# Optimization experiments

Measured on AMD Instinct MI355X. Metric: run time of the kernel, lower is better.

The kernel has to match this reference:

```python
import jax, jax.numpy as jnp
import numpy as np

S, B, D, H, A = 256, 1024, 64, 128, 8  # seq_len, buffer, state_size, hidden, action_size


def _init(key, shape, fan_in):
    bound = 1.0 / np.sqrt(fan_in)
    return jax.random.uniform(key, shape, jnp.float32, -bound, bound)


def setup_inputs() -> dict:
    key = jax.random.key(0)
    ks = jax.random.split(key, 24)
    inp = {"state": jax.random.normal(ks[0], (S, B, D), jnp.float32)}
    # actor / critic MLPs (Linear(D,H) + ReLU + Linear(H,H) + ReLU)
    inp["aw1"] = _init(ks[1], (H, D), D); inp["ab1"] = _init(ks[2], (H,), D)
    inp["aw2"] = _init(ks[3], (H, H), H); inp["ab2"] = _init(ks[4], (H,), H)
    inp["cw1"] = _init(ks[5], (H, D), D); inp["cb1"] = _init(ks[6], (H,), D)
    inp["cw2"] = _init(ks[7], (H, H), H); inp["cb2"] = _init(ks[8], (H,), H)
    # LSTMs (PyTorch layout: W_ih [4H,H], W_hh [4H,H], gate order i,f,g,o)
    inp["a_wih"] = _init(ks[9], (4 * H, H), H); inp["a_whh"] = _init(ks[10], (4 * H, H), H)
    inp["a_bih"] = _init(ks[11], (4 * H,), H); inp["a_bhh"] = _init(ks[12], (4 * H,), H)
    inp["c_wih"] = _init(ks[13], (4 * H, H), H); inp["c_whh"] = _init(ks[14], (4 * H, H), H)
    inp["c_bih"] = _init(ks[15], (4 * H,), H); inp["c_bhh"] = _init(ks[16], (4 * H,), H)
    # heads
    inp["mw"] = _init(ks[17], (A, H), H); inp["mb"] = _init(ks[18], (A,), H)
    inp["lw"] = _init(ks[19], (A, H), H); inp["lb"] = _init(ks[20], (A,), H)
    inp["vw"] = _init(ks[21], (1, H), H); inp["vb"] = _init(ks[22], (1,), H)
    return inp


def _mlp(x, w1, b1, w2, b2):
    h = jax.nn.relu(jnp.einsum('sbd,hd->sbh', x, w1) + b1)
    return jax.nn.relu(jnp.einsum('sbh,gh->sbg', h, w2) + b2)


def _lstm_zero_state(x, w_ih, b_ih, b_hh):
    # Each timestep runs with fresh zero (h, c): the recurrent term vanishes,
    # so the whole sequence is one batched GEMM + gating (W_hh unused).
    gates = jnp.einsum('sbh,gh->sbg', x, w_ih) + b_ih + b_hh  # [S,B,4H]
    i, f, g, o = jnp.split(gates, 4, axis=-1)
    c = jax.nn.sigmoid(i) * jnp.tanh(g)  # f * c_prev = 0
    return jax.nn.sigmoid(o) * jnp.tanh(c)


def reference(state, aw1, ab1, aw2, ab2, cw1, cb1, cw2, cb2,
              a_wih, a_whh, a_bih, a_bhh, c_wih, c_whh, c_bih, c_bhh,
              mw, mb, lw, lb, vw, vb):
    actor_h = _lstm_zero_state(_mlp(state, aw1, ab1, aw2, ab2), a_wih, a_bih, a_bhh)
    critic_h = _lstm_zero_state(_mlp(state, cw1, cb1, cw2, cb2), c_wih, c_bih, c_bhh)
    mean = jnp.einsum('sbh,ah->sba', actor_h, mw) + mb
    std = jnp.exp(jnp.einsum('sbh,ah->sba', actor_h, lw) + lb)
    value = jnp.einsum('sbh,vh->sbv', critic_h, vw) + vb
    return (mean, std, value)
```

## Files before the change

kernel.cpp:

```cpp
#include <hip/hip_runtime.h>


#define NROWS (256 * 1024)
#define HID 128
#define ACTD 8

#define W1_OFF 0
#define W2_OFF 16384
#define WI_OFF 49152
#define WG_OFF 81920
#define WO_OFF 114688
#define PSTR 147456
#define HEAD_OFF (2 * PSTR)
#define GB_OFF (HEAD_OFF + 8192)

#define NEG_L (-1.4426950408889634f)
#define TWO_L (2.8853900817779268f)

typedef __attribute__((ext_vector_type(8))) short s16x8;
typedef __attribute__((ext_vector_type(4))) float fx4;
typedef __attribute__((ext_vector_type(2))) unsigned int u32x2;
typedef __attribute__((ext_vector_type(4))) unsigned int u32x4;

__device__ __forceinline__ unsigned int cvtpk(float lo, float hi) {
  unsigned int r;
  asm("v_cvt_pk_bf16_f32 %0, %1, %2" : "=v"(r) : "v"(lo), "v"(hi));
  return r;
}

__device__ __forceinline__ float ex2(float x) {
  return __builtin_amdgcn_exp2f(x);
}
__device__ __forceinline__ float frcp(float x) {
  return __builtin_amdgcn_rcpf(x);
}

__device__ __forceinline__ s16x8 frag_ld(const unsigned short* base, int row,
                                         int kbyte, int rowsh) {
  int byte = (row << rowsh) + (kbyte ^ ((row & 7) << 4));
  return *(const s16x8*)((const char*)base + byte);
}

__device__ __forceinline__ void zacc(fx4 acc[4][2]) {
#pragma unroll
  for (int j = 0; j < 4; ++j)
#pragma unroll
    for (int i = 0; i < 2; ++i) acc[j][i] = fx4{0.f, 0.f, 0.f, 0.f};
}

__device__ __forceinline__ void bacc(fx4 acc[4][2], const float* __restrict__ b,
                                     int fb, int g4) {
#pragma unroll
  for (int it = 0; it < 2; ++it) {
    fx4 bv = *(const fx4*)(b + fb + it * 16 + g4);
#pragma unroll
    for (int jt = 0; jt < 4; ++jt) acc[jt][it] = bv;
  }
}

template <int KC, int ASH>
__device__ __forceinline__ void gemm_g(const char* __restrict__ wimg,
                                       const unsigned short* at, int wv,
                                       int lane, fx4 acc[4][2]) {
  const int l15 = lane & 15;
  const int kb0 = (lane >> 4) << 4;
  const int woff = ((lane >> 4) << 8) + (l15 << 4);
#pragma unroll
  for (int kc = 0; kc < KC; ++kc) {
    int kbyte = kc * 64 + kb0;
    s16x8 w0 = *(const s16x8*)(wimg + (((wv * 2 + 0) * KC + kc) << 10) + woff);
    s16x8 w1 = *(const s16x8*)(wimg + (((wv * 2 + 1) * KC + kc) << 10) + woff);
#pragma unroll
    for (int jt = 0; jt < 4; ++jt) {
      s16x8 a = frag_ld(at, jt * 16 + l15, kbyte, ASH);
      acc[jt][0] = __builtin_amdgcn_mfma_f32_16x16x32_bf16(w0, a, acc[jt][0], 0, 0, 0);
      acc[jt][1] = __builtin_amdgcn_mfma_f32_16x16x32_bf16(w1, a, acc[jt][1], 0, 0, 0);
    }
  }
}

__device__ __forceinline__ void epi_relu(fx4 acc[4][2], unsigned short* obuf,
                                         int fb, int lane) {
  const int g4 = (lane >> 4) << 2;
  const int l15 = lane & 15;
  char* ob = (char*)obuf;
#pragma unroll
  for (int it = 0; it < 2; ++it) {
    int n0 = fb + it * 16 + g4;
#pragma unroll
    for (int jt = 0; jt < 4; ++jt) {
      fx4 v = acc[jt][it];
#pragma unroll
      for (int r = 0; r < 4; ++r) v[r] = fmaxf(v[r], 0.0f);
      u32x2 u;
      u[0] = cvtpk(v[0], v[1]);
      u[1] = cvtpk(v[2], v[3]);
      int m = jt * 16 + l15;
      *(u32x2*)(ob + (m << 8) + ((n0 * 2) ^ ((m & 7) << 4))) = u;
    }
  }
}

__global__ void prep_weights(const float* __restrict__ aw1,
                             const float* __restrict__ aw2,
                             const float* __restrict__ awih,
                             const float* __restrict__ cw1,
                             const float* __restrict__ cw2,
                             const float* __restrict__ cwih,
                             const float* __restrict__ mw,
                             const float* __restrict__ lw,
                             const float* __restrict__ vw,
                             const float* __restrict__ abih,
                             const float* __restrict__ abhh,
                             const float* __restrict__ cbih,
                             const float* __restrict__ cbhh,
                             char* __restrict__ ws) {
  int y = blockIdx.y;
  int idx = blockIdx.x * 256 + threadIdx.x;
  if (y >= 12) {
    if (idx < 384) {
      float* dst = (float*)(ws + GB_OFF + (size_t)(y - 12) * 1536);
      const float* b0 = (y == 12) ? abih : cbih;
      const float* b1 = (y == 12) ? abhh : cbhh;
      int sect = idx >> 7, f = idx & 127;
      int srow = (sect == 0) ? f : (sect == 1) ? 256 + f : 384 + f;
      float scale = (sect == 1) ? TWO_L : NEG_L;
      dst[idx] = scale * (b0[srow] + b1[srow]);
    }
    return;
  }
  if (y >= 10) {
    if (idx >= 256) return;
    int row = idx >> 4, c16 = idx & 15, kc = c16 >> 2, ks = c16 & 3;
    fx4 v0 = {0.f, 0.f, 0.f, 0.f}, v1 = v0;
    if (y == 10) {
      const float* src = (row < 8) ? (mw + (size_t)row * HID + c16 * 8)
                                   : (lw + (size_t)(row - 8) * HID + c16 * 8);
      v0 = ((const fx4*)src)[0];
      v1 = ((const fx4*)src)[1];
    } else if (row == 0) {
      const float* src = vw + c16 * 8;
      v0 = ((const fx4*)src)[0];
      v1 = ((const fx4*)src)[1];
    }
    u32x4 u;
    u[0] = cvtpk(v0[0], v0[1]);
    u[1] = cvtpk(v0[2], v0[3]);
    u[2] = cvtpk(v1[0], v1[1]);
    u[3] = cvtpk(v1[2], v1[3]);
    int dst = ((kc * 4 + ks) * 16 + row) * 16;
    *(u32x4*)(ws + HEAD_OFF + (size_t)(y - 10) * 4096 + dst) = u;
    return;
  }
  const float* src;
  int nch, ksh, KC, off;
  switch (y) {
    case 0:  src = aw1;              nch = 1024; ksh = 3; KC = 2; off = W1_OFF;        break;
    case 1:  src = aw2;              nch = 2048; ksh = 4; KC = 4; off = W2_OFF;        break;
    case 2:  src = awih;             nch = 2048; ksh = 4; KC = 4; off = WI_OFF;        break;
    case 3:  src = awih + 256 * HID; nch = 2048; ksh = 4; KC = 4; off = WG_OFF;        break;
    case 4:  src = awih + 384 * HID; nch = 2048; ksh = 4; KC = 4; off = WO_OFF;        break;
    case 5:  src = cw1;              nch = 1024; ksh = 3; KC = 2; off = PSTR + W1_OFF; break;
    case 6:  src = cw2;              nch = 2048; ksh = 4; KC = 4; off = PSTR + W2_OFF; break;
    case 7:  src = cwih;             nch = 2048; ksh = 4; KC = 4; off = PSTR + WI_OFF; break;
    case 8:  src = cwih + 256 * HID; nch = 2048; ksh = 4; KC = 4; off = PSTR + WG_OFF; break;
    default: src = cwih + 384 * HID; nch = 2048; ksh = 4; KC = 4; off = PSTR + WO_OFF; break;
  }
  if (idx >= nch) return;
  int row = idx >> ksh;
  int c16 = idx & ((1 << ksh) - 1);
  int b2 = row >> 4, r = row & 15, kc = c16 >> 2, ks = c16 & 3;
  const fx4* gp = (const fx4*)(src + (size_t)idx * 8);
  fx4 v0 = gp[0], v1 = gp[1];
  u32x4 u;
  u[0] = cvtpk(v0[0], v0[1]);
  u[1] = cvtpk(v0[2], v0[3]);
  u[2] = cvtpk(v1[0], v1[1]);
  u[3] = cvtpk(v1[2], v1[3]);
  int dst = (((b2 * KC + kc) * 4 + ks) * 16 + r) * 16;
  *(u32x4*)(ws + off + dst) = u;
}

__global__ __launch_bounds__(256, 3) void fused_ac(
    const float* __restrict__ state, const float* __restrict__ ab1,
    const float* __restrict__ ab2, const float* __restrict__ cb1,
    const float* __restrict__ cb2, const float* __restrict__ mb,
    const float* __restrict__ lb, const float* __restrict__ vb,
    const char* __restrict__ ws, float* __restrict__ outp) {
  __shared__ __align__(16) unsigned short abuf[8192];

  const int tid = threadIdx.x;
  const int lane = tid & 63;
  const int wv = tid >> 6;
  const int l15 = lane & 15;
  const int g4 = (lane >> 4) << 2;
  const int kb0 = (lane >> 4) << 4;
  const int fb = wv << 5;
  const int path = blockIdx.x >> 12;
  const int rbase = (blockIdx.x & 4095) << 6;

  const char* wsp = ws + (size_t)path * PSTR;
  const float* b1 = path ? cb1 : ab1;
  const float* b2 = path ? cb2 : ab2;
  const float* gb = (const float*)(ws + GB_OFF + (size_t)path * 1536);
  const char* himg = ws + HEAD_OFF + (size_t)path * 4096;

  float* meanp = outp;
  float* stdp = outp + (size_t)NROWS * ACTD;
  float* valp = outp + (size_t)NROWS * ACTD * 2;

  {
    const float* xg = state + (size_t)rbase * 64;
    char* ab = (char*)abuf;
#pragma unroll
    for (int i = 0; i < 2; ++i) {
      int idx = tid + i * 256;
      int r = idx >> 3, c = idx & 7;
      const fx4* gp = (const fx4*)(xg + idx * 8);
      fx4 v0 = gp[0], v1 = gp[1];
      u32x4 u;
      u[0] = cvtpk(v0[0], v0[1]);
      u[1] = cvtpk(v0[2], v0[3]);
      u[2] = cvtpk(v1[0], v1[1]);
      u[3] = cvtpk(v1[2], v1[3]);
      *(u32x4*)(ab + r * 128 + ((c << 4) ^ ((r & 7) << 4))) = u;
    }
  }
  __syncthreads();

  fx4 acc[4][2];
  bacc(acc, b1, fb, g4);
  gemm_g<2, 7>(wsp + W1_OFF, abuf, wv, lane, acc);
  __syncthreads();
  epi_relu(acc, abuf, fb, lane);
  __syncthreads();

  bacc(acc, b2, fb, g4);
  gemm_g<4, 8>(wsp + W2_OFF, abuf, wv, lane, acc);
  __syncthreads();
  epi_relu(acc, abuf, fb, lane);
  __syncthreads();

  fx4 carry[4][2];
  zacc(acc);
  gemm_g<4, 8>(wsp + WI_OFF, abuf, wv, lane, acc);
#pragma unroll
  for (int it = 0; it < 2; ++it) {
    fx4 pv = *(const fx4*)(gb + fb + it * 16 + g4);
#pragma unroll
    for (int jt = 0; jt < 4; ++jt)
#pragma unroll
      for (int r = 0; r < 4; ++r)
        carry[jt][it][r] = ex2(fmaf(acc[jt][it][r], NEG_L, pv[r]));
  }

  zacc(acc);
  gemm_g<4, 8>(wsp + WG_OFF, abuf, wv, lane, acc);
#pragma unroll
  for (int it = 0; it < 2; ++it) {
    fx4 pv = *(const fx4*)(gb + 128 + fb + it * 16 + g4);
#pragma unroll
    for (int jt = 0; jt < 4; ++jt)
#pragma unroll
      for (int r = 0; r < 4; ++r) {
        float Eg = ex2(fmaf(acc[jt][it][r], TWO_L, pv[r]));
        float c = (Eg - 1.0f) * frcp((Eg + 1.0f) * (carry[jt][it][r] + 1.0f));
        carry[jt][it][r] = ex2(c * TWO_L);
      }
  }

  zacc(acc);
  gemm_g<4, 8>(wsp + WO_OFF, abuf, wv, lane, acc);
  __syncthreads();
  {
    char* ob = (char*)abuf;
#pragma unroll
    for (int it = 0; it < 2; ++it) {
      fx4 pv = *(const fx4*)(gb + 256 + fb + it * 16 + g4);
      int n0 = fb + it * 16 + g4;
#pragma unroll
      for (int jt = 0; jt < 4; ++jt) {
        fx4 h;
#pragma unroll
        for (int r = 0; r < 4; ++r) {
          float Eo = ex2(fmaf(acc[jt][it][r], NEG_L, pv[r]));
          float Ec = carry[jt][it][r];
          h[r] = (Ec - 1.0f) * frcp((Ec + 1.0f) * (Eo + 1.0f));
        }
        u32x2 u;
        u[0] = cvtpk(h[0], h[1]);
        u[1] = cvtpk(h[2], h[3]);
        int m = jt * 16 + l15;
        *(u32x2*)(ob + (m << 8) + ((n0 * 2) ^ ((m & 7) << 4))) = u;
      }
    }
  }
  __syncthreads();

  fx4 ha = fx4{0.f, 0.f, 0.f, 0.f};
  const int woff = ((lane >> 4) << 8) + (l15 << 4);
#pragma unroll
  for (int kc = 0; kc < 4; ++kc) {
    s16x8 w = *(const s16x8*)(himg + (kc << 10) + woff);
    s16x8 a = frag_ld(abuf, (wv << 4) + l15, kc * 64 + kb0, 8);
    ha = __builtin_amdgcn_mfma_f32_16x16x32_bf16(w, a, ha, 0, 0, 0);
  }

  int m = rbase + (wv << 4) + l15;
  if (path == 0) {
    if (g4 < 8) {
      fx4 v = ha + *(const fx4*)(mb + g4);
      *(fx4*)(meanp + (size_t)m * ACTD + g4) = v;
    } else {
      fx4 v;
#pragma unroll
      for (int r = 0; r < 4; ++r) v[r] = __expf(ha[r] + lb[g4 - 8 + r]);
      *(fx4*)(stdp + (size_t)m * ACTD + (g4 - 8)) = v;
    }
  } else if (g4 == 0) {
    valp[m] = ha[0] + vb[0];
  }
}

extern "C" void kernel_launch(void* const* d_in, const int* in_sizes, int n_in,
                              void* d_out, int out_size, void* d_ws,
                              size_t ws_size, hipStream_t stream) {
  (void)in_sizes; (void)n_in; (void)ws_size; (void)out_size;
  const float* state = (const float*)d_in[0];
  const float* aw1 = (const float*)d_in[1];
  const float* ab1 = (const float*)d_in[2];
  const float* aw2 = (const float*)d_in[3];
  const float* ab2 = (const float*)d_in[4];
  const float* cw1 = (const float*)d_in[5];
  const float* cb1 = (const float*)d_in[6];
  const float* cw2 = (const float*)d_in[7];
  const float* cb2 = (const float*)d_in[8];
  const float* awih = (const float*)d_in[9];
  const float* abih = (const float*)d_in[11];
  const float* abhh = (const float*)d_in[12];
  const float* cwih = (const float*)d_in[13];
  const float* cbih = (const float*)d_in[15];
  const float* cbhh = (const float*)d_in[16];
  const float* mw = (const float*)d_in[17];
  const float* mb = (const float*)d_in[18];
  const float* lw = (const float*)d_in[19];
  const float* lb = (const float*)d_in[20];
  const float* vw = (const float*)d_in[21];
  const float* vb = (const float*)d_in[22];
  char* ws = (char*)d_ws;

  prep_weights<<<dim3(8, 14), 256, 0, stream>>>(
      aw1, aw2, awih, cw1, cw2, cwih, mw, lw, vw, abih, abhh, cbih, cbhh, ws);
  fused_ac<<<8192, 256, 0, stream>>>(state, ab1, ab2, cb1, cb2, mb, lb, vb, ws,
                                     (float*)d_out);
}
```

Measured before the change: 125.6 us.

## Double-buffer LDS activations and prefetch weight fragments ahead of GEMMs

Adds a second shared-memory buffer so each layer's epilogue writes into the buffer the next GEMM does not read. This removes two of the __syncthreads barriers around each MLP layer and the one before the final hidden-state store. Weight fragments for the next GEMM stage and the head are loaded from global memory before the preceding epilogue, to hide load latency. The cost is doubled LDS per block (32KB) and more live registers, which could reduce occupancy relative to the launch_bounds target of 3 blocks.

```diff
diff --git a/kernel.cpp b/kernel.cpp
--- a/kernel.cpp
+++ b/kernel.cpp
@@ -27,7 +27,6 @@
   asm("v_cvt_pk_bf16_f32 %0, %1, %2" : "=v"(r) : "v"(lo), "v"(hi));
   return r;
 }
-
 __device__ __forceinline__ float ex2(float x) {
   return __builtin_amdgcn_exp2f(x);
 }
@@ -41,13 +40,36 @@
   return *(const s16x8*)((const char*)base + byte);
 }
 
+struct wpair {
+  s16x8 w0, w1;
+};
+template <int KC>
+__device__ __forceinline__ wpair wload(const char* __restrict__ wimg, int wv,
+                                       int kc, int woff) {
+  wpair p;
+  p.w0 = *(const s16x8*)(wimg + (((wv * 2 + 0) * KC + kc) << 10) + woff);
+  p.w1 = *(const s16x8*)(wimg + (((wv * 2 + 1) * KC + kc) << 10) + woff);
+  return p;
+}
+
+template <int ASH>
+__device__ __forceinline__ void gemm_kc(const wpair& p,
+                                        const unsigned short* at, int kbyte,
+                                        int l15, fx4 acc[4][2]) {
+#pragma unroll
+  for (int jt = 0; jt < 4; ++jt) {
+    s16x8 a = frag_ld(at, jt * 16 + l15, kbyte, ASH);
+    acc[jt][0] = __builtin_amdgcn_mfma_f32_16x16x32_bf16(p.w0, a, acc[jt][0], 0, 0, 0);
+    acc[jt][1] = __builtin_amdgcn_mfma_f32_16x16x32_bf16(p.w1, a, acc[jt][1], 0, 0, 0);
+  }
+}
+
 __device__ __forceinline__ void zacc(fx4 acc[4][2]) {
 #pragma unroll
   for (int j = 0; j < 4; ++j)
 #pragma unroll
     for (int i = 0; i < 2; ++i) acc[j][i] = fx4{0.f, 0.f, 0.f, 0.f};
 }
-
 __device__ __forceinline__ void bacc(fx4 acc[4][2], const float* __restrict__ b,
                                      int fb, int g4) {
 #pragma unroll
@@ -55,27 +77,6 @@
     fx4 bv = *(const fx4*)(b + fb + it * 16 + g4);
 #pragma unroll
     for (int jt = 0; jt < 4; ++jt) acc[jt][it] = bv;
-  }
-}
-
-template <int KC, int ASH>
-__device__ __forceinline__ void gemm_g(const char* __restrict__ wimg,
-                                       const unsigned short* at, int wv,
-                                       int lane, fx4 acc[4][2]) {
-  const int l15 = lane & 15;
-  const int kb0 = (lane >> 4) << 4;
-  const int woff = ((lane >> 4) << 8) + (l15 << 4);
-#pragma unroll
-  for (int kc = 0; kc < KC; ++kc) {
-    int kbyte = kc * 64 + kb0;
-    s16x8 w0 = *(const s16x8*)(wimg + (((wv * 2 + 0) * KC + kc) << 10) + woff);
-    s16x8 w1 = *(const s16x8*)(wimg + (((wv * 2 + 1) * KC + kc) << 10) + woff);
-#pragma unroll
-    for (int jt = 0; jt < 4; ++jt) {
-      s16x8 a = frag_ld(at, jt * 16 + l15, kbyte, ASH);
-      acc[jt][0] = __builtin_amdgcn_mfma_f32_16x16x32_bf16(w0, a, acc[jt][0], 0, 0, 0);
-      acc[jt][1] = __builtin_amdgcn_mfma_f32_16x16x32_bf16(w1, a, acc[jt][1], 0, 0, 0);
-    }
   }
 }
 
@@ -188,6 +189,7 @@
     const float* __restrict__ lb, const float* __restrict__ vb,
     const char* __restrict__ ws, float* __restrict__ outp) {
   __shared__ __align__(16) unsigned short abuf[8192];
+  __shared__ __align__(16) unsigned short hbuf[8192];
 
   const int tid = threadIdx.x;
   const int lane = tid & 63;
@@ -195,6 +197,7 @@
   const int l15 = lane & 15;
   const int g4 = (lane >> 4) << 2;
   const int kb0 = (lane >> 4) << 4;
+  const int woff = ((lane >> 4) << 8) + (l15 << 4);
   const int fb = wv << 5;
   const int path = blockIdx.x >> 12;
   const int rbase = (blockIdx.x & 4095) << 6;
@@ -208,6 +211,9 @@
   float* meanp = outp;
   float* stdp = outp + (size_t)NROWS * ACTD;
   float* valp = outp + (size_t)NROWS * ACTD * 2;
+
+  wpair w1a = wload<2>(wsp + W1_OFF, wv, 0, woff);
+  wpair w1b = wload<2>(wsp + W1_OFF, wv, 1, woff);
 
   {
     const float* xg = state + (size_t)rbase * 64;
@@ -230,20 +236,41 @@
 
   fx4 acc[4][2];
   bacc(acc, b1, fb, g4);
-  gemm_g<2, 7>(wsp + W1_OFF, abuf, wv, lane, acc);
+  gemm_kc<7>(w1a, abuf, 0 + kb0, l15, acc);
+  gemm_kc<7>(w1b, abuf, 64 + kb0, l15, acc);
+  wpair w2a = wload<4>(wsp + W2_OFF, wv, 0, woff);
+  wpair w2b = wload<4>(wsp + W2_OFF, wv, 1, woff);
+  epi_relu(acc, hbuf, fb, lane);
   __syncthreads();
+
+  bacc(acc, b2, fb, g4);
+  gemm_kc<8>(w2a, hbuf, 0 + kb0, l15, acc);
+  gemm_kc<8>(w2b, hbuf, 64 + kb0, l15, acc);
+  {
+    wpair p = wload<4>(wsp + W2_OFF, wv, 2, woff);
+    gemm_kc<8>(p, hbuf, 128 + kb0, l15, acc);
+  }
+  {
+    wpair p = wload<4>(wsp + W2_OFF, wv, 3, woff);
+    gemm_kc<8>(p, hbuf, 192 + kb0, l15, acc);
+  }
+  wpair wia = wload<4>(wsp + WI_OFF, wv, 0, woff);
+  wpair wib = wload<4>(wsp + WI_OFF, wv, 1, woff);
   epi_relu(acc, abuf, fb, lane);
   __syncthreads();
 
-  bacc(acc, b2, fb, g4);
-  gemm_g<4, 8>(wsp + W2_OFF, abuf, wv, lane, acc);
-  __syncthreads();
-  epi_relu(acc, abuf, fb, lane);
-  __syncthreads();
-
   fx4 carry[4][2];
   zacc(acc);
-  gemm_g<4, 8>(wsp + WI_OFF, abuf, wv, lane, acc);
+  gemm_kc<8>(wia, abuf, 0 + kb0, l15, acc);
+  gemm_kc<8>(wib, abuf, 64 + kb0, l15, acc);
+  {
+    wpair p = wload<4>(wsp + WI_OFF, wv, 2, woff);
+    gemm_kc<8>(p, abuf, 128 + kb0, l15, acc);
+  }
+  {
+    wpair p = wload<4>(wsp + WI_OFF, wv, 3, woff);
+    gemm_kc<8>(p, abuf, 192 + kb0, l15, acc);
+  }
 #pragma unroll
   for (int it = 0; it < 2; ++it) {
     fx4 pv = *(const fx4*)(gb + fb + it * 16 + g4);
@@ -255,7 +282,11 @@
   }
 
   zacc(acc);
-  gemm_g<4, 8>(wsp + WG_OFF, abuf, wv, lane, acc);
+#pragma unroll
+  for (int kc = 0; kc < 4; ++kc) {
+    wpair p = wload<4>(wsp + WG_OFF, wv, kc, woff);
+    gemm_kc<8>(p, abuf, kc * 64 + kb0, l15, acc);
+  }
 #pragma unroll
   for (int it = 0; it < 2; ++it) {
     fx4 pv = *(const fx4*)(gb + 128 + fb + it * 16 + g4);
@@ -270,10 +301,17 @@
   }
 
   zacc(acc);
-  gemm_g<4, 8>(wsp + WO_OFF, abuf, wv, lane, acc);
-  __syncthreads();
-  {
-    char* ob = (char*)abuf;
+#pragma unroll
+  for (int kc = 0; kc < 4; ++kc) {
+    wpair p = wload<4>(wsp + WO_OFF, wv, kc, woff);
+    gemm_kc<8>(p, abuf, kc * 64 + kb0, l15, acc);
+  }
+  s16x8 hw0 = *(const s16x8*)(himg + (0 << 10) + woff);
+  s16x8 hw1 = *(const s16x8*)(himg + (1 << 10) + woff);
+  s16x8 hw2 = *(const s16x8*)(himg + (2 << 10) + woff);
+  s16x8 hw3 = *(const s16x8*)(himg + (3 << 10) + woff);
+  {
+    char* ob = (char*)hbuf;
 #pragma unroll
     for (int it = 0; it < 2; ++it) {
       fx4 pv = *(const fx4*)(gb + 256 + fb + it * 16 + g4);
@@ -298,13 +336,14 @@
   __syncthreads();
 
   fx4 ha = fx4{0.f, 0.f, 0.f, 0.f};
-  const int woff = ((lane >> 4) << 8) + (l15 << 4);
-#pragma unroll
-  for (int kc = 0; kc < 4; ++kc) {
-    s16x8 w = *(const s16x8*)(himg + (kc << 10) + woff);
-    s16x8 a = frag_ld(abuf, (wv << 4) + l15, kc * 64 + kb0, 8);
-    ha = __builtin_amdgcn_mfma_f32_16x16x32_bf16(w, a, ha, 0, 0, 0);
-  }
+  ha = __builtin_amdgcn_mfma_f32_16x16x32_bf16(
+      hw0, frag_ld(hbuf, (wv << 4) + l15, 0 + kb0, 8), ha, 0, 0, 0);
+  ha = __builtin_amdgcn_mfma_f32_16x16x32_bf16(
+      hw1, frag_ld(hbuf, (wv << 4) + l15, 64 + kb0, 8), ha, 0, 0, 0);
+  ha = __builtin_amdgcn_mfma_f32_16x16x32_bf16(
+      hw2, frag_ld(hbuf, (wv << 4) + l15, 128 + kb0, 8), ha, 0, 0, 0);
+  ha = __builtin_amdgcn_mfma_f32_16x16x32_bf16(
+      hw3, frag_ld(hbuf, (wv << 4) + l15, 192 + kb0, 8), ha, 0, 0, 0);
 
   int m = rbase + (wv << 4) + l15;
   if (path == 0) {
```

Measured after the change: 120.1 us. 4.4% less time.
